# Optimization experiments

Hardware: AMD Instinct MI355X
Metric: run time of the kernel (lower is better)

The kernel has to match this reference:

```python
import jax, jax.numpy as jnp
import numpy as np

B, T, C, FFN, N_LAYER, LAYER_ID = 4, 2048, 1024, 4096, 24, 1
EPS = 1e-5


def setup_inputs() -> dict:
    key = jax.random.key(0)
    ks = jax.random.split(key, 10)
    scale = 0.02

    def w(k, shape):
        return (jax.random.normal(k, shape, jnp.float32) * scale)

    # RWKV-4 init formulas for layer_id=1, n_layer=24 (learned params, init per source)
    r01 = LAYER_ID / (N_LAYER - 1)
    r10 = 1.0 - LAYER_ID / N_LAYER
    ddd = np.arange(C, dtype=np.float64) / C
    h = np.arange(C, dtype=np.float64)
    decay = -5.0 + 8.0 * (h / (C - 1)) ** (0.7 + 1.3 * r01)
    zigzag = np.array([(i + 1) % 3 - 1 for i in range(C)], dtype=np.float64) * 0.5
    tfirst = np.log(0.3) + zigzag

    return {
        "x": jax.random.normal(ks[0], (B, T, C), jnp.float32),
        "ln1_w": jnp.ones((C,), jnp.float32), "ln1_b": jnp.zeros((C,), jnp.float32),
        "ln2_w": jnp.ones((C,), jnp.float32), "ln2_b": jnp.zeros((C,), jnp.float32),
        "time_decay": jnp.asarray(decay, jnp.float32),
        "time_first": jnp.asarray(tfirst, jnp.float32),
        "tmk": jnp.asarray(ddd ** r10, jnp.float32),
        "tmv": jnp.asarray(ddd ** r10 + 0.3 * r01, jnp.float32),
        "tmr": jnp.asarray(ddd ** (0.5 * r10), jnp.float32),
        "att_kw": w(ks[1], (C, C)), "att_vw": w(ks[2], (C, C)),
        "att_rw": w(ks[3], (C, C)), "att_ow": w(ks[4], (C, C)),
        "f_tmk": jnp.asarray(ddd ** r10, jnp.float32),
        "f_tmr": jnp.asarray(ddd ** r10, jnp.float32),
        "f_kw": w(ks[5], (FFN, C)), "f_rw": w(ks[6], (C, C)), "f_vw": w(ks[7], (C, FFN)),
    }


def _ln(z, g, b):
    m = jnp.mean(z, axis=-1, keepdims=True)
    v = jnp.mean(jnp.square(z - m), axis=-1, keepdims=True)
    return (z - m) * jax.lax.rsqrt(v + EPS) * g + b


def _shift(z):  # token shift: prepend zero row along T, drop last
    return jnp.pad(z, ((0, 0), (1, 0), (0, 0)))[:, :-1]


def _wkv(time_decay, u, k, v):
    # Numerically-stable RWKV-4 WKV recurrence (log-space max trick).
    # k, v: [B, T, C]; time_decay, u: [C]
    w = -jnp.exp(time_decay)  # per-channel decay (negative)
    kt = jnp.moveaxis(k, 1, 0)  # [T, B, C]
    vt = jnp.moveaxis(v, 1, 0)
    aa = jnp.zeros_like(kt[0])
    bb = jnp.zeros_like(kt[0])
    pp = jnp.full_like(kt[0], -1e38)

    def step(carry, kv):
        aa, bb, pp = carry
        kk, vv = kv
        ww = u + kk
        p = jnp.maximum(pp, ww)
        e1 = jnp.exp(pp - p)
        e2 = jnp.exp(ww - p)
        out = (e1 * aa + e2 * vv) / (e1 * bb + e2)
        ww2 = pp + w
        p2 = jnp.maximum(ww2, kk)
        e1b = jnp.exp(ww2 - p2)
        e2b = jnp.exp(kk - p2)
        return (e1b * aa + e2b * vv, e1b * bb + e2b, p2), out

    _, out = jax.lax.scan(step, (aa, bb, pp), (kt, vt))
    return jnp.moveaxis(out, 0, 1)  # [B, T, C]


def reference(x, ln1_w, ln1_b, ln2_w, ln2_b, time_decay, time_first,
              tmk, tmv, tmr, att_kw, att_vw, att_rw, att_ow,
              f_tmk, f_tmr, f_kw, f_rw, f_vw):
    # --- RWKV_TimeMix (layer_id != 0; protectors are identity in fwd for finite vals) ---
    h = _ln(x, ln1_w, ln1_b)
    hx = _shift(h)
    xk = h * tmk + hx * (1.0 - tmk)
    xv = h * tmv + hx * (1.0 - tmv)
    xr = h * tmr + hx * (1.0 - tmr)
    k = jnp.einsum('btc,dc->btd', xk, att_kw)
    v = jnp.einsum('btc,dc->btd', xv, att_vw)
    sr = jax.nn.sigmoid(jnp.einsum('btc,dc->btd', xr, att_rw))
    rwkv = sr * _wkv(time_decay, time_first, k, v)
    x = x + jnp.einsum('btd,cd->btc', rwkv, att_ow)
    # --- RWKV_ChannelMix ---
    h = _ln(x, ln2_w, ln2_b)
    hx = _shift(h)
    xk = h * f_tmk + hx * (1.0 - f_tmk)
    xr = h * f_tmr + hx * (1.0 - f_tmr)
    kk = jnp.square(jax.nn.relu(jnp.einsum('btc,fc->btf', xk, f_kw)))
    kv = jnp.einsum('btf,cf->btc', kk, f_vw)
    x = x + jax.nn.sigmoid(jnp.einsum('btc,dc->btd', xr, f_rw)) * kv
    return x
```

## Files before the change

### kernel.cpp

```cpp
#include <hip/hip_runtime.h>
#include <cstdint>

#define C_DIM 1024
#define T_DIM 2048
#define B_DIM 4
#define FFN_DIM 4096
#define NROWS (B_DIM * T_DIM)
#define NELEM ((size_t)NROWS * C_DIM)
#define MB ((size_t)1 << 20)
#define NSEG 32
#define SEGL (T_DIM / NSEG)

typedef __bf16 bf16;
typedef __bf16 bf16x4 __attribute__((ext_vector_type(4)));
typedef __bf16 bf16x8 __attribute__((ext_vector_type(8)));
typedef float  floatx4 __attribute__((ext_vector_type(4)));

#define GLDS(g, l) __builtin_amdgcn_global_load_lds(                          \
    (const __attribute__((address_space(1))) void*)(g),                       \
    (__attribute__((address_space(3))) void*)(l), 16, 0, 0)

__device__ __forceinline__ void store_out(float* p, float v) { *p = v; }
__device__ __forceinline__ void store_out(bf16* p, float v)  { *p = (bf16)v; }

struct W7 {
    const float* s[7];
    bf16*        d[7];
    int          cum[8];
};

__global__ __launch_bounds__(256) void f2b7_kernel(W7 w)
{
    int id = blockIdx.x * 256 + threadIdx.x;
    int seg = 0;
#pragma unroll
    for (int j = 1; j < 7; ++j) if (id >= w.cum[j]) seg = j;
    int i = id - w.cum[seg];
    float4 v = ((const float4*)w.s[seg])[i];
    bf16x4 o = { (bf16)v.x, (bf16)v.y, (bf16)v.z, (bf16)v.w };
    ((bf16x4*)w.d[seg])[i] = o;
}

template<bool HASV>
__global__ __launch_bounds__(256) void lnmix_kernel(const float* __restrict__ x,
                                                    const float* __restrict__ g,
                                                    const float* __restrict__ b,
                                                    const float* __restrict__ mk,
                                                    const float* __restrict__ mv,
                                                    const float* __restrict__ mr,
                                                    bf16* __restrict__ xk,
                                                    bf16* __restrict__ xv,
                                                    bf16* __restrict__ xr)
{
    int row = blockIdx.x;
    int t   = row & (T_DIM - 1);
    int tid = threadIdx.x;
    size_t i4 = (size_t)row * 256 + tid;

    float4 v  = ((const float4*)x)[i4];
    float4 vp = make_float4(0.f, 0.f, 0.f, 0.f);
    if (t != 0) vp = ((const float4*)x)[i4 - 256];

    float s   = v.x + v.y + v.z + v.w;
    float s2  = v.x * v.x + v.y * v.y + v.z * v.z + v.w * v.w;
    float sp  = vp.x + vp.y + vp.z + vp.w;
    float sp2 = vp.x * vp.x + vp.y * vp.y + vp.z * vp.z + vp.w * vp.w;
    for (int off = 32; off > 0; off >>= 1) {
        s   += __shfl_down(s,   off);
        s2  += __shfl_down(s2,  off);
        sp  += __shfl_down(sp,  off);
        sp2 += __shfl_down(sp2, off);
    }
    __shared__ float red[16];
    int lane = tid & 63, wid = tid >> 6;
    if (lane == 0) { red[wid] = s; red[4 + wid] = s2; red[8 + wid] = sp; red[12 + wid] = sp2; }
    __syncthreads();
    s   = red[0] + red[1] + red[2] + red[3];
    s2  = red[4] + red[5] + red[6] + red[7];
    sp  = red[8] + red[9] + red[10] + red[11];
    sp2 = red[12] + red[13] + red[14] + red[15];

    float mean  = s * (1.0f / C_DIM);
    float inv   = rsqrtf(s2 * (1.0f / C_DIM) - mean * mean + 1e-5f);
    float meanp = sp * (1.0f / C_DIM);
    float invp  = rsqrtf(sp2 * (1.0f / C_DIM) - meanp * meanp + 1e-5f);

    float4 gv = ((const float4*)g)[tid];
    float4 bv = ((const float4*)b)[tid];
    float4 hv, hp;
    hv.x = (v.x - mean) * inv * gv.x + bv.x;
    hv.y = (v.y - mean) * inv * gv.y + bv.y;
    hv.z = (v.z - mean) * inv * gv.z + bv.z;
    hv.w = (v.w - mean) * inv * gv.w + bv.w;
    if (t != 0) {
        hp.x = (vp.x - meanp) * invp * gv.x + bv.x;
        hp.y = (vp.y - meanp) * invp * gv.y + bv.y;
        hp.z = (vp.z - meanp) * invp * gv.z + bv.z;
        hp.w = (vp.w - meanp) * invp * gv.w + bv.w;
    } else {
        hp = make_float4(0.f, 0.f, 0.f, 0.f);
    }

    float4 m1 = ((const float4*)mk)[tid];
    bf16x4 o;
    o.x = (bf16)(hp.x + m1.x * (hv.x - hp.x));
    o.y = (bf16)(hp.y + m1.y * (hv.y - hp.y));
    o.z = (bf16)(hp.z + m1.z * (hv.z - hp.z));
    o.w = (bf16)(hp.w + m1.w * (hv.w - hp.w));
    ((bf16x4*)xk)[i4] = o;

    if (HASV) {
        float4 m2 = ((const float4*)mv)[tid];
        o.x = (bf16)(hp.x + m2.x * (hv.x - hp.x));
        o.y = (bf16)(hp.y + m2.y * (hv.y - hp.y));
        o.z = (bf16)(hp.z + m2.z * (hv.z - hp.z));
        o.w = (bf16)(hp.w + m2.w * (hv.w - hp.w));
        ((bf16x4*)xv)[i4] = o;
    }

    float4 m3 = ((const float4*)mr)[tid];
    o.x = (bf16)(hp.x + m3.x * (hv.x - hp.x));
    o.y = (bf16)(hp.y + m3.y * (hv.y - hp.y));
    o.z = (bf16)(hp.z + m3.z * (hv.z - hp.z));
    o.w = (bf16)(hp.w + m3.w * (hv.w - hp.w));
    ((bf16x4*)xr)[i4] = o;
}

#define EPI_NONE 0
#define EPI_SIG 1
#define EPI_RELU2 2
#define EPI_ADD 3
#define EPI_SCALEADD 4

template<int EPI, typename OutT>
__global__ __launch_bounds__(256) void gemm_bf16(const bf16* __restrict__ A,
                                                 const bf16* __restrict__ W,
                                                 OutT* __restrict__ Y,
                                                 const float* __restrict__ X2,
                                                 const bf16* __restrict__ S,
                                                 int N, int K)
{
    __shared__ unsigned short As[128 * 32];
    __shared__ unsigned short Bs[128 * 32];

    int tid = threadIdx.x;
    int ntn    = N >> 7;
    int stride = ntn >> 3;
    int id  = blockIdx.x;
    int sq  = id >> 3;
    int n_t = (id & 7) * stride + (sq % stride);
    int m_t = sq / stride;
    int m0 = m_t * 128, n0 = n_t * 128;

    int r0  = tid >> 2;
    int qsw = ((tid & 3) - ((r0 >> 1) & 3)) & 3;
    const bf16* Ag = A + (size_t)(m0 + r0) * K + qsw * 8;
    const bf16* Wg = W + (size_t)(n0 + r0) * K + qsw * 8;
    size_t rowK = (size_t)64 * K;
    int wv = tid >> 6;
    unsigned short* AsW0 = As + wv * 512;
    unsigned short* AsW1 = As + 2048 + wv * 512;
    unsigned short* BsW0 = Bs + wv * 512;
    unsigned short* BsW1 = Bs + 2048 + wv * 512;

    int ln = tid & 63;
    int wm = (wv & 1) * 64, wn = (wv >> 1) * 64;
    int ra0 = wm + (ln & 15);
    int rb0 = wn + (ln & 15);
    int qa  = ln >> 4;
    int abase = ra0 * 32 + (((qa + (ra0 >> 1)) & 3) * 8);
    int bbase = rb0 * 32 + (((qa + (rb0 >> 1)) & 3) * 8);

    floatx4 acc[4][4] = {};

    for (int k0 = 0; k0 < K; k0 += 32) {
        if (k0) __syncthreads();
        GLDS(Ag + k0,        AsW0);
        GLDS(Ag + k0 + rowK, AsW1);
        GLDS(Wg + k0,        BsW0);
        GLDS(Wg + k0 + rowK, BsW1);
        __syncthreads();

        bf16x8 a[4], b[4];
#pragma unroll
        for (int i = 0; i < 4; ++i) a[i] = *(const bf16x8*)(As + abase + i * 512);
#pragma unroll
        for (int j = 0; j < 4; ++j) b[j] = *(const bf16x8*)(Bs + bbase + j * 512);
#pragma unroll
        for (int i = 0; i < 4; ++i)
#pragma unroll
            for (int j = 0; j < 4; ++j)
                acc[i][j] = __builtin_amdgcn_mfma_f32_16x16x32_bf16(a[i], b[j], acc[i][j], 0, 0, 0);
    }

    int row0 = (ln >> 4) * 4;
    int colb = n0 + wn + (ln & 15);
#pragma unroll
    for (int i = 0; i < 4; ++i) {
        int gm = m0 + wm + i * 16 + row0;
#pragma unroll
        for (int j = 0; j < 4; ++j) {
            int gn = colb + j * 16;
#pragma unroll
            for (int r = 0; r < 4; ++r) {
                size_t idx = (size_t)(gm + r) * N + gn;
                float v = acc[i][j][r];
                if (EPI == EPI_SIG)        v = 1.0f / (1.0f + __expf(-v));
                else if (EPI == EPI_RELU2) { float t = fmaxf(v, 0.0f); v = t * t; }
                else if (EPI == EPI_ADD)   v = X2[idx] + v;
                else if (EPI == EPI_SCALEADD) v = X2[idx] + (float)S[idx] * v;
                store_out(&Y[idx], v);
            }
        }
    }
}

__global__ __launch_bounds__(256) void wkv_seg(const float* __restrict__ k,
                                               const float* __restrict__ v,
                                               const float* __restrict__ decay,
                                               float* __restrict__ sa,
                                               float* __restrict__ sb,
                                               float* __restrict__ sp)
{
    int idx = blockIdx.x * 256 + threadIdx.x;
    int c   = idx & (C_DIM - 1);
    int bs  = idx >> 10;
    int seg = bs & (NSEG - 1);
    int b   = bs >> 5;
    float w = -__expf(decay[c]);
    size_t base = ((size_t)b * T_DIM + (size_t)seg * SEGL) * C_DIM + c;
    float aa = 0.f, bb = 0.f, pp = -1e38f;
    for (int t = 0; t < SEGL; ++t) {
        size_t off = base + (size_t)t * C_DIM;
        float kk = k[off], vv = v[off];
        float ww2 = pp + w;
        float p2  = fmaxf(ww2, kk);
        float e1  = __expf(ww2 - p2);
        float e2  = __expf(kk - p2);
        aa = e1 * aa + e2 * vv;
        bb = e1 * bb + e2;
        pp = p2;
    }
    sa[idx] = aa; sb[idx] = bb; sp[idx] = pp;
}

__global__ __launch_bounds__(256) void wkv_comb(const float* __restrict__ sa,
                                                const float* __restrict__ sb,
                                                const float* __restrict__ sp,
                                                const float* __restrict__ decay,
                                                float* __restrict__ ia,
                                                float* __restrict__ ib,
                                                float* __restrict__ ip)
{
    int idx = blockIdx.x * 256 + threadIdx.x;
    int c = idx & (C_DIM - 1);
    int b = idx >> 10;
    float wL = -__expf(decay[c]) * (float)SEGL;
    float aa = 0.f, bb = 0.f, pp = -1e38f;
    size_t base = (size_t)b * NSEG * C_DIM + c;
    for (int j = 0; j < NSEG; ++j) {
        size_t o = base + (size_t)j * C_DIM;
        ia[o] = aa; ib[o] = bb; ip[o] = pp;
        float a_s = sa[o], b_s = sb[o], p_s = sp[o];
        float pd = pp + wL;
        float pn = fmaxf(pd, p_s);
        float e1 = __expf(pd - pn);
        float e2 = __expf(p_s - pn);
        aa = e1 * aa + e2 * a_s;
        bb = e1 * bb + e2 * b_s;
        pp = pn;
    }
}

__global__ __launch_bounds__(256) void wkv_out(const float* __restrict__ k,
                                               const float* __restrict__ v,
                                               const bf16* __restrict__ sr,
                                               const float* __restrict__ decay,
                                               const float* __restrict__ first,
                                               const float* __restrict__ ia,
                                               const float* __restrict__ ib,
                                               const float* __restrict__ ip,
                                               bf16* __restrict__ out)
{
    int idx = blockIdx.x * 256 + threadIdx.x;
    int c   = idx & (C_DIM - 1);
    int bs  = idx >> 10;
    int seg = bs & (NSEG - 1);
    int b   = bs >> 5;
    float w = -__expf(decay[c]);
    float u = first[c];
    float aa = ia[idx], bb = ib[idx], pp = ip[idx];
    size_t base = ((size_t)b * T_DIM + (size_t)seg * SEGL) * C_DIM + c;
    for (int t = 0; t < SEGL; ++t) {
        size_t off = base + (size_t)t * C_DIM;
        float kk = k[off], vv = v[off];
        float ww = u + kk;
        float p  = fmaxf(pp, ww);
        float e1 = __expf(pp - p);
        float e2 = __expf(ww - p);
        float o  = (e1 * aa + e2 * vv) / (e1 * bb + e2);
        out[off] = (bf16)((float)sr[off] * o);
        float ww2 = pp + w;
        float p2  = fmaxf(ww2, kk);
        float e1b = __expf(ww2 - p2);
        float e2b = __expf(kk - p2);
        aa = e1b * aa + e2b * vv;
        bb = e1b * bb + e2b;
        pp = p2;
    }
}

extern "C" void kernel_launch(void* const* d_in, const int* in_sizes, int n_in,
                              void* d_out, int out_size, void* d_ws, size_t ws_size,
                              hipStream_t stream)
{
    const float* x          = (const float*)d_in[0];
    const float* ln1_w      = (const float*)d_in[1];
    const float* ln1_b      = (const float*)d_in[2];
    const float* ln2_w      = (const float*)d_in[3];
    const float* ln2_b      = (const float*)d_in[4];
    const float* time_decay = (const float*)d_in[5];
    const float* time_first = (const float*)d_in[6];
    const float* tmk        = (const float*)d_in[7];
    const float* tmv        = (const float*)d_in[8];
    const float* tmr        = (const float*)d_in[9];
    const float* att_kw     = (const float*)d_in[10];
    const float* att_vw     = (const float*)d_in[11];
    const float* att_rw     = (const float*)d_in[12];
    const float* att_ow     = (const float*)d_in[13];
    const float* f_tmk      = (const float*)d_in[14];
    const float* f_tmr      = (const float*)d_in[15];
    const float* f_kw       = (const float*)d_in[16];
    const float* f_rw       = (const float*)d_in[17];
    const float* f_vw       = (const float*)d_in[18];
    float* out = (float*)d_out;

    char* W8 = (char*)d_ws;
    bf16* kw_b  = (bf16*)(W8 + 0 * MB);
    bf16* vw_b  = (bf16*)(W8 + 2 * MB);
    bf16* rw_b  = (bf16*)(W8 + 4 * MB);
    bf16* ow_b  = (bf16*)(W8 + 6 * MB);
    bf16* fkw_b = (bf16*)(W8 + 8 * MB);
    bf16* frw_b = (bf16*)(W8 + 16 * MB);
    bf16* fvw_b = (bf16*)(W8 + 18 * MB);

    bf16*  xk_b   = (bf16*)(W8 + 26 * MB);
    bf16*  xv_b   = (bf16*)(W8 + 42 * MB);
    bf16*  xr_b   = (bf16*)(W8 + 58 * MB);
    bf16*  rwkv_b = xk_b;
    bf16*  xk2_b  = (bf16*)(W8 + 26 * MB);
    bf16*  xr2_b  = (bf16*)(W8 + 42 * MB);
    bf16*  sr2_b  = (bf16*)(W8 + 58 * MB);
    float* kbuf   = (float*)(W8 + 74 * MB);
    float* vbuf   = (float*)(W8 + 106 * MB);
    bf16*  srb_b  = (bf16*)(W8 + 138 * MB);
    bf16*  kk_b   = (bf16*)(W8 + 106 * MB);

    size_t KB512 = (size_t)512 * 1024;
    float* sc_a = (float*)(W8 + 170 * MB);
    float* sc_b = (float*)(W8 + 170 * MB + 1 * KB512);
    float* sc_p = (float*)(W8 + 170 * MB + 2 * KB512);
    float* in_a = (float*)(W8 + 170 * MB + 3 * KB512);
    float* in_b = (float*)(W8 + 170 * MB + 4 * KB512);
    float* in_p = (float*)(W8 + 170 * MB + 5 * KB512);

    int nC4 = C_DIM * C_DIM / 4, nF4 = FFN_DIM * C_DIM / 4;
    W7 w7;
    const float* srcs[7] = { att_kw, att_vw, att_rw, att_ow, f_kw, f_rw, f_vw };
    bf16*        dsts[7] = { kw_b, vw_b, rw_b, ow_b, fkw_b, frw_b, fvw_b };
    int          cnts[7] = { nC4, nC4, nC4, nC4, nF4, nC4, nF4 };
    int cum = 0;
    for (int i = 0; i < 7; ++i) { w7.s[i] = srcs[i]; w7.d[i] = dsts[i]; w7.cum[i] = cum; cum += cnts[i]; }
    w7.cum[7] = cum;
    f2b7_kernel<<<cum / 256, 256, 0, stream>>>(w7);

    dim3 gC(8 * 64);
    dim3 gF(32 * 64);
    int segGrid = B_DIM * NSEG * C_DIM / 256;

    lnmix_kernel<true><<<NROWS, 256, 0, stream>>>(x, ln1_w, ln1_b, tmk, tmv, tmr,
                                                  xk_b, xv_b, xr_b);
    gemm_bf16<EPI_NONE, float><<<gC, 256, 0, stream>>>(xk_b, kw_b, kbuf, nullptr, nullptr, C_DIM, C_DIM);
    gemm_bf16<EPI_NONE, float><<<gC, 256, 0, stream>>>(xv_b, vw_b, vbuf, nullptr, nullptr, C_DIM, C_DIM);
    gemm_bf16<EPI_SIG,  bf16 ><<<gC, 256, 0, stream>>>(xr_b, rw_b, srb_b, nullptr, nullptr, C_DIM, C_DIM);
    wkv_seg<<<segGrid, 256, 0, stream>>>(kbuf, vbuf, time_decay, sc_a, sc_b, sc_p);
    wkv_comb<<<B_DIM * C_DIM / 256, 256, 0, stream>>>(sc_a, sc_b, sc_p, time_decay, in_a, in_b, in_p);
    wkv_out<<<segGrid, 256, 0, stream>>>(kbuf, vbuf, srb_b, time_decay, time_first,
                                         in_a, in_b, in_p, rwkv_b);
    gemm_bf16<EPI_ADD,  float><<<gC, 256, 0, stream>>>(rwkv_b, ow_b, out, x, nullptr, C_DIM, C_DIM);

    lnmix_kernel<false><<<NROWS, 256, 0, stream>>>(out, ln2_w, ln2_b, f_tmk, nullptr, f_tmr,
                                                   xk2_b, nullptr, xr2_b);
    gemm_bf16<EPI_SIG,   bf16><<<gC, 256, 0, stream>>>(xr2_b, frw_b, sr2_b, nullptr, nullptr, C_DIM, C_DIM);
    gemm_bf16<EPI_RELU2, bf16><<<gF, 256, 0, stream>>>(xk2_b, fkw_b, kk_b, nullptr, nullptr, FFN_DIM, C_DIM);
    gemm_bf16<EPI_SCALEADD, float><<<gC, 256, 0, stream>>>(kk_b, fvw_b, out, out, sr2_b, C_DIM, FFN_DIM);
}
```

Baseline: 562.4 us.

## Group independent GEMMs into single launches and store k/v in fp16

Replaces the templated GEMM with one grouped kernel that takes up to four GEMM descriptors, so the k/v/r projections and the FFN r/k projections each run as a single launch. The epilogue and output type are now chosen at runtime instead of by template. The k and v projections are written as fp16 instead of fp32, which halves the traffic those buffers cause in the WKV kernels. The tile mapping across XCDs is also reworked. Risks include runtime branching in the epilogue, fp16 range and precision limits on k and v, and a new tile mapping that hardcodes 64 M-tiles.

```diff
diff --git a/kernel.cpp b/kernel.cpp
--- a/kernel.cpp
+++ b/kernel.cpp
@@ -12,6 +12,7 @@
 #define SEGL (T_DIM / NSEG)
 
 typedef __bf16 bf16;
+typedef _Float16 f16;
 typedef __bf16 bf16x4 __attribute__((ext_vector_type(4)));
 typedef __bf16 bf16x8 __attribute__((ext_vector_type(8)));
 typedef float  floatx4 __attribute__((ext_vector_type(4)));
@@ -19,9 +20,6 @@
 #define GLDS(g, l) __builtin_amdgcn_global_load_lds(                          \
     (const __attribute__((address_space(1))) void*)(g),                       \
     (__attribute__((address_space(3))) void*)(l), 16, 0, 0)
-
-__device__ __forceinline__ void store_out(float* p, float v) { *p = v; }
-__device__ __forceinline__ void store_out(bf16* p, float v)  { *p = (bf16)v; }
 
 struct W7 {
     const float* s[7];
@@ -132,26 +130,37 @@
 #define EPI_ADD 3
 #define EPI_SCALEADD 4
 
-template<int EPI, typename OutT>
-__global__ __launch_bounds__(256) void gemm_bf16(const bf16* __restrict__ A,
-                                                 const bf16* __restrict__ W,
-                                                 OutT* __restrict__ Y,
-                                                 const float* __restrict__ X2,
-                                                 const bf16* __restrict__ S,
-                                                 int N, int K)
+struct GArgs {
+    const bf16*  A[4];
+    const bf16*  W[4];
+    void*        Y[4];
+    const float* X2[4];
+    const bf16*  S[4];
+    int N[4], K[4], epi[4], outk[4], blk0[4];
+    int ng;
+};
+
+__global__ __launch_bounds__(256) void gemm_grouped(GArgs G)
 {
     __shared__ unsigned short As[128 * 32];
     __shared__ unsigned short Bs[128 * 32];
 
+    int id = blockIdx.x;
+    int gi = 0;
+#pragma unroll
+    for (int j = 1; j < 4; ++j) if (j < G.ng && id >= G.blk0[j]) gi = j;
+
+    const bf16* A = G.A[gi];
+    const bf16* W = G.W[gi];
+    int N = G.N[gi], K = G.K[gi];
+    int lid = id - G.blk0[gi];
+
+    int xcd = lid & 7, r = lid >> 3;
+    int m_t = xcd * 8 + (r & 7);
+    int n_t = r >> 3;
+    int m0 = m_t << 7, n0 = n_t << 7;
+
     int tid = threadIdx.x;
-    int ntn    = N >> 7;
-    int stride = ntn >> 3;
-    int id  = blockIdx.x;
-    int sq  = id >> 3;
-    int n_t = (id & 7) * stride + (sq % stride);
-    int m_t = sq / stride;
-    int m0 = m_t * 128, n0 = n_t * 128;
-
     int r0  = tid >> 2;
     int qsw = ((tid & 3) - ((r0 >> 1) & 3)) & 3;
     const bf16* Ag = A + (size_t)(m0 + r0) * K + qsw * 8;
@@ -193,6 +202,13 @@
                 acc[i][j] = __builtin_amdgcn_mfma_f32_16x16x32_bf16(a[i], b[j], acc[i][j], 0, 0, 0);
     }
 
+    int epi = G.epi[gi], outk = G.outk[gi];
+    const float* X2 = G.X2[gi];
+    const bf16*  S  = G.S[gi];
+    float* Yf = (float*)G.Y[gi];
+    bf16*  Yh = (bf16*)G.Y[gi];
+    f16*   Ye = (f16*)G.Y[gi];
+
     int row0 = (ln >> 4) * 4;
     int colb = n0 + wn + (ln & 15);
 #pragma unroll
@@ -202,21 +218,23 @@
         for (int j = 0; j < 4; ++j) {
             int gn = colb + j * 16;
 #pragma unroll
-            for (int r = 0; r < 4; ++r) {
-                size_t idx = (size_t)(gm + r) * N + gn;
-                float v = acc[i][j][r];
-                if (EPI == EPI_SIG)        v = 1.0f / (1.0f + __expf(-v));
-                else if (EPI == EPI_RELU2) { float t = fmaxf(v, 0.0f); v = t * t; }
-                else if (EPI == EPI_ADD)   v = X2[idx] + v;
-                else if (EPI == EPI_SCALEADD) v = X2[idx] + (float)S[idx] * v;
-                store_out(&Y[idx], v);
+            for (int rr = 0; rr < 4; ++rr) {
+                size_t idx = (size_t)(gm + rr) * N + gn;
+                float v = acc[i][j][rr];
+                if (epi == EPI_SIG)        v = 1.0f / (1.0f + __expf(-v));
+                else if (epi == EPI_RELU2) { float t = fmaxf(v, 0.0f); v = t * t; }
+                else if (epi == EPI_ADD)   v = X2[idx] + v;
+                else if (epi == EPI_SCALEADD) v = X2[idx] + (float)S[idx] * v;
+                if (outk == 0)      Yf[idx] = v;
+                else if (outk == 1) Yh[idx] = (bf16)v;
+                else                Ye[idx] = (f16)v;
             }
         }
     }
 }
 
-__global__ __launch_bounds__(256) void wkv_seg(const float* __restrict__ k,
-                                               const float* __restrict__ v,
+__global__ __launch_bounds__(256) void wkv_seg(const f16* __restrict__ k,
+                                               const f16* __restrict__ v,
                                                const float* __restrict__ decay,
                                                float* __restrict__ sa,
                                                float* __restrict__ sb,
@@ -232,7 +250,7 @@
     float aa = 0.f, bb = 0.f, pp = -1e38f;
     for (int t = 0; t < SEGL; ++t) {
         size_t off = base + (size_t)t * C_DIM;
-        float kk = k[off], vv = v[off];
+        float kk = (float)k[off], vv = (float)v[off];
         float ww2 = pp + w;
         float p2  = fmaxf(ww2, kk);
         float e1  = __expf(ww2 - p2);
@@ -272,8 +290,8 @@
     }
 }
 
-__global__ __launch_bounds__(256) void wkv_out(const float* __restrict__ k,
-                                               const float* __restrict__ v,
+__global__ __launch_bounds__(256) void wkv_out(const f16* __restrict__ k,
+                                               const f16* __restrict__ v,
                                                const bf16* __restrict__ sr,
                                                const float* __restrict__ decay,
                                                const float* __restrict__ first,
@@ -293,7 +311,7 @@
     size_t base = ((size_t)b * T_DIM + (size_t)seg * SEGL) * C_DIM + c;
     for (int t = 0; t < SEGL; ++t) {
         size_t off = base + (size_t)t * C_DIM;
-        float kk = k[off], vv = v[off];
+        float kk = (float)k[off], vv = (float)v[off];
         float ww = u + kk;
         float p  = fmaxf(pp, ww);
         float e1 = __expf(pp - p);
@@ -351,18 +369,18 @@
     bf16*  xk2_b  = (bf16*)(W8 + 26 * MB);
     bf16*  xr2_b  = (bf16*)(W8 + 42 * MB);
     bf16*  sr2_b  = (bf16*)(W8 + 58 * MB);
-    float* kbuf   = (float*)(W8 + 74 * MB);
-    float* vbuf   = (float*)(W8 + 106 * MB);
-    bf16*  srb_b  = (bf16*)(W8 + 138 * MB);
-    bf16*  kk_b   = (bf16*)(W8 + 106 * MB);
+    f16*   kbuf   = (f16*)(W8 + 74 * MB);
+    f16*   vbuf   = (f16*)(W8 + 90 * MB);
+    bf16*  srb_b  = (bf16*)(W8 + 106 * MB);
+    bf16*  kk_b   = (bf16*)(W8 + 122 * MB);
 
     size_t KB512 = (size_t)512 * 1024;
-    float* sc_a = (float*)(W8 + 170 * MB);
-    float* sc_b = (float*)(W8 + 170 * MB + 1 * KB512);
-    float* sc_p = (float*)(W8 + 170 * MB + 2 * KB512);
-    float* in_a = (float*)(W8 + 170 * MB + 3 * KB512);
-    float* in_b = (float*)(W8 + 170 * MB + 4 * KB512);
-    float* in_p = (float*)(W8 + 170 * MB + 5 * KB512);
+    float* sc_a = (float*)(W8 + 186 * MB);
+    float* sc_b = (float*)(W8 + 186 * MB + 1 * KB512);
+    float* sc_p = (float*)(W8 + 186 * MB + 2 * KB512);
+    float* in_a = (float*)(W8 + 186 * MB + 3 * KB512);
+    float* in_b = (float*)(W8 + 186 * MB + 4 * KB512);
+    float* in_p = (float*)(W8 + 186 * MB + 5 * KB512);
 
     int nC4 = C_DIM * C_DIM / 4, nF4 = FFN_DIM * C_DIM / 4;
     W7 w7;
@@ -374,24 +392,46 @@
     w7.cum[7] = cum;
     f2b7_kernel<<<cum / 256, 256, 0, stream>>>(w7);
 
-    dim3 gC(8 * 64);
-    dim3 gF(32 * 64);
+    auto mkdesc = [](GArgs& G, int& total, const bf16* A, const bf16* W, void* Y,
+                     const float* X2, const bf16* S, int N, int K, int epi, int outk) {
+        int i = G.ng;
+        G.A[i] = A; G.W[i] = W; G.Y[i] = Y; G.X2[i] = X2; G.S[i] = S;
+        G.N[i] = N; G.K[i] = K; G.epi[i] = epi; G.outk[i] = outk;
+        G.blk0[i] = total; total += 64 * (N >> 7); G.ng = i + 1;
+    };
+
     int segGrid = B_DIM * NSEG * C_DIM / 256;
 
     lnmix_kernel<true><<<NROWS, 256, 0, stream>>>(x, ln1_w, ln1_b, tmk, tmv, tmr,
                                                   xk_b, xv_b, xr_b);
-    gemm_bf16<EPI_NONE, float><<<gC, 256, 0, stream>>>(xk_b, kw_b, kbuf, nullptr, nullptr, C_DIM, C_DIM);
-    gemm_bf16<EPI_NONE, float><<<gC, 256, 0, stream>>>(xv_b, vw_b, vbuf, nullptr, nullptr, C_DIM, C_DIM);
-    gemm_bf16<EPI_SIG,  bf16 ><<<gC, 256, 0, stream>>>(xr_b, rw_b, srb_b, nullptr, nullptr, C_DIM, C_DIM);
+    {
+        GArgs G = {}; int total = 0;
+        mkdesc(G, total, xk_b, kw_b, kbuf,  nullptr, nullptr, C_DIM, C_DIM, EPI_NONE, 2);
+        mkdesc(G, total, xv_b, vw_b, vbuf,  nullptr, nullptr, C_DIM, C_DIM, EPI_NONE, 2);
+        mkdesc(G, total, xr_b, rw_b, srb_b, nullptr, nullptr, C_DIM, C_DIM, EPI_SIG,  1);
+        gemm_grouped<<<total, 256, 0, stream>>>(G);
+    }
     wkv_seg<<<segGrid, 256, 0, stream>>>(kbuf, vbuf, time_decay, sc_a, sc_b, sc_p);
     wkv_comb<<<B_DIM * C_DIM / 256, 256, 0, stream>>>(sc_a, sc_b, sc_p, time_decay, in_a, in_b, in_p);
     wkv_out<<<segGrid, 256, 0, stream>>>(kbuf, vbuf, srb_b, time_decay, time_first,
                                          in_a, in_b, in_p, rwkv_b);
-    gemm_bf16<EPI_ADD,  float><<<gC, 256, 0, stream>>>(rwkv_b, ow_b, out, x, nullptr, C_DIM, C_DIM);
+    {
+        GArgs G = {}; int total = 0;
+        mkdesc(G, total, rwkv_b, ow_b, out, x, nullptr, C_DIM, C_DIM, EPI_ADD, 0);
+        gemm_grouped<<<total, 256, 0, stream>>>(G);
+    }
 
     lnmix_kernel<false><<<NROWS, 256, 0, stream>>>(out, ln2_w, ln2_b, f_tmk, nullptr, f_tmr,
                                                    xk2_b, nullptr, xr2_b);
-    gemm_bf16<EPI_SIG,   bf16><<<gC, 256, 0, stream>>>(xr2_b, frw_b, sr2_b, nullptr, nullptr, C_DIM, C_DIM);
-    gemm_bf16<EPI_RELU2, bf16><<<gF, 256, 0, stream>>>(xk2_b, fkw_b, kk_b, nullptr, nullptr, FFN_DIM, C_DIM);
-    gemm_bf16<EPI_SCALEADD, float><<<gC, 256, 0, stream>>>(kk_b, fvw_b, out, out, sr2_b, C_DIM, FFN_DIM);
-}
+    {
+        GArgs G = {}; int total = 0;
+        mkdesc(G, total, xr2_b, frw_b, sr2_b, nullptr, nullptr, C_DIM,   C_DIM, EPI_SIG,   1);
+        mkdesc(G, total, xk2_b, fkw_b, kk_b,  nullptr, nullptr, FFN_DIM, C_DIM, EPI_RELU2, 1);
+        gemm_grouped<<<total, 256, 0, stream>>>(G);
+    }
+    {
+        GArgs G = {}; int total = 0;
+        mkdesc(G, total, kk_b, fvw_b, out, out, sr2_b, C_DIM, FFN_DIM, EPI_SCALEADD, 0);
+        gemm_grouped<<<total, 256, 0, stream>>>(G);
+    }
+}
```

After: 589.0 us. 1.05x slower.
